# Optimization experiments

Measured on AMD Instinct MI355X. Metric: run time of the kernel, lower is better.

## Reference

```python
import jax, jax.numpy as jnp
import numpy as np

H = 256          # hidden_dim
E = 2 * H        # encoder output / attention embed dim = 512
MEL = 512        # mel_dim (must equal E for the original attention call to type-check)
NH = 8
HD = E // NH     # 64
B = 16
T = 128
V = 256          # vocab_size
NSPK = 100       # hardcoded speaker embedding rows
MAX_LEN = min(1000, T * 10)  # 1000 decode steps


def setup_inputs() -> dict:
    key = jax.random.key(0)
    ks = iter(jax.random.split(key, 40))

    def w(shape, s=0.05):
        return jax.random.normal(next(ks), shape, dtype=jnp.float32) * s

    return {
        'text_tokens': jax.random.randint(next(ks), (B, T), 0, V),
        'speaker_id': jax.random.randint(next(ks), (B,), 0, NSPK),
        'emb_text': w((V, H)),
        'emb_speaker': w((NSPK, H)),
        # bidirectional encoder LSTM (PyTorch gate order i,f,g,o)
        'enc_f_Wih': w((4 * H, H)), 'enc_f_Whh': w((4 * H, H)),
        'enc_f_bih': w((4 * H,)), 'enc_f_bhh': w((4 * H,)),
        'enc_b_Wih': w((4 * H, H)), 'enc_b_Whh': w((4 * H, H)),
        'enc_b_bih': w((4 * H,)), 'enc_b_bhh': w((4 * H,)),
        # multihead attention in/out projections
        'Wq': w((E, E)), 'bq': w((E,)),
        'Wk': w((E, E)), 'bk': w((E,)),
        'Wv': w((E, E)), 'bv': w((E,)),
        'Wo': w((E, E)), 'bo': w((E,)),
        # decoder LSTM (input dim = E + MEL); hidden state is re-zeroed every
        # step in the original (output state discarded), so Whh never acts.
        'dec_Wih': w((4 * H, E + MEL)), 'dec_Whh': w((4 * H, H)),
        'dec_bih': w((4 * H,)), 'dec_bhh': w((4 * H,)),
        'Wmel': w((MEL, H)), 'bmel': w((MEL,)),
        'Wstop': w((1, H)), 'bstop': w((1,)),
    }


def _lstm(x, Wih, Whh, bih, bhh, reverse=False):
    # x: [B, T, D] -> hidden sequence [B, T, H]
    Bx = x.shape[0]
    Hh = Whh.shape[1]
    h0 = jnp.zeros((Bx, Hh), x.dtype)

    def step(carry, xt):
        h, c = carry
        gates = xt @ Wih.T + bih + h @ Whh.T + bhh
        i, f, g, o = jnp.split(gates, 4, axis=-1)
        c = jax.nn.sigmoid(f) * c + jax.nn.sigmoid(i) * jnp.tanh(g)
        h = jax.nn.sigmoid(o) * jnp.tanh(c)
        return (h, c), h

    _, hs = jax.lax.scan(step, (h0, h0), jnp.swapaxes(x, 0, 1), reverse=reverse)
    return jnp.swapaxes(hs, 0, 1)


def reference(text_tokens, speaker_id, emb_text, emb_speaker,
              enc_f_Wih, enc_f_Whh, enc_f_bih, enc_f_bhh,
              enc_b_Wih, enc_b_Whh, enc_b_bih, enc_b_bhh,
              Wq, bq, Wk, bk, Wv, bv, Wo, bo,
              dec_Wih, dec_Whh, dec_bih, dec_bhh,
              Wmel, bmel, Wstop, bstop):
    # text + speaker embedding
    x = emb_text[text_tokens] + emb_speaker[speaker_id][:, None, :]   # [B,T,H]
    # bidirectional LSTM encoder
    enc_f = _lstm(x, enc_f_Wih, enc_f_Whh, enc_f_bih, enc_f_bhh)
    enc_b = _lstm(x, enc_b_Wih, enc_b_Whh, enc_b_bih, enc_b_bhh, reverse=True)
    enc = jnp.concatenate([enc_f, enc_b], axis=-1)                    # [B,T,E]

    # K/V projections are constant across decode steps -> hoist out of the loop
    K = (enc @ Wk.T + bk).reshape(B, T, NH, HD).transpose(0, 2, 1, 3)   # [B,NH,T,HD]
    Vv = (enc @ Wv.T + bv).reshape(B, T, NH, HD).transpose(0, 2, 1, 3)  # [B,NH,T,HD]
    scale = 1.0 / np.sqrt(HD).astype(np.float32)

    def step(mel_in, _):
        # single-query multihead attention (query = previous mel frame)
        q = (mel_in @ Wq.T + bq).reshape(B, NH, HD)                     # [B,NH,HD]
        w = jax.nn.softmax(jnp.einsum('bhd,bhtd->bht', q, K) * scale, axis=-1)
        ctx = jnp.einsum('bht,bhtd->bhd', w, Vv).reshape(B, E)
        attended = ctx @ Wo.T + bo                                      # [B,E]
        xin = jnp.concatenate([attended, mel_in], axis=-1)              # [B,E+MEL]
        # decoder LSTM single step from ZERO state each step (state discarded
        # in the original), so Whh term vanishes
        gates = xin @ dec_Wih.T + dec_bih + dec_bhh
        i, f, g, o = jnp.split(gates, 4, axis=-1)
        c = jax.nn.sigmoid(i) * jnp.tanh(g)
        h = jax.nn.sigmoid(o) * jnp.tanh(c)                             # [B,H]
        mel = h @ Wmel.T + bmel                                         # [B,MEL]
        stop = h @ Wstop.T + bstop                                      # [B,1]
        return mel, (mel, stop, w.mean(axis=1))

    mel0 = jnp.zeros((B, MEL), jnp.float32)
    _, (mels, stops, attns) = jax.lax.scan(step, mel0, None, length=MAX_LEN)

    mel_output = jnp.swapaxes(mels, 0, 1)    # [B,MAX_LEN,MEL]
    stop_output = jnp.swapaxes(stops, 0, 1)  # [B,MAX_LEN,1]
    attn_last = attns[-1][:, None, :]        # [B,1,T] (head-averaged, last step)
    return mel_output, stop_output, attn_last
```

## Files before the change

### kernel.cpp

```cpp
#include <hip/hip_runtime.h>
#include <hip/hip_bf16.h>


typedef unsigned short u16;
typedef unsigned int   u32;
#define DI __device__ __forceinline__

static constexpr size_t WS_BAR   = 0;
static constexpr size_t WS_GBUF  = 64*1024;
static constexpr size_t WS_HBUF  = 192*1024;
static constexpr size_t WS_PROBS = 208*1024;
static constexpr size_t WS_BIAS  = 272*1024;
static constexpr size_t WS_W2M   = 320*1024;
static constexpr size_t WS_WQH   = 832*1024;
static constexpr size_t WS_WCG   = 1344*1024;

static constexpr size_t OF_ENC_A = 262144;
static constexpr size_t OF_ENC_B = 1286144;
static constexpr size_t OF_XWF   = 4015744;
static constexpr size_t OF_XWB   = 6112896;

DI float bf2f(u16 u){ union{u32 i; float f;} v; v.i = ((u32)u)<<16; return v.f; }
DI u16 f2bf(float f){ union{float f; u32 i;} v; v.f = f;
  u32 r = v.i + 0x7fffu + ((v.i>>16)&1u); return (u16)(r>>16); }
DI float2 bf2x(u32 u){ union{u32 i; float f;} a,b; a.i = u<<16; b.i = u & 0xffff0000u;
  float2 r; r.x = a.f; r.y = b.f; return r; }
DI float dot8(uint4 wv, float4 a, float4 b){
  float2 w0 = bf2x(wv.x), w1 = bf2x(wv.y), w2 = bf2x(wv.z), w3 = bf2x(wv.w);
  return w0.x*a.x + w0.y*a.y + w1.x*a.z + w1.y*a.w
       + w2.x*b.x + w2.y*b.y + w3.x*b.z + w3.y*b.w;
}
DI float dot8f(float4 wa, float4 wb, float4 a, float4 b){
  return wa.x*a.x + wa.y*a.y + wa.z*a.z + wa.w*a.w
       + wb.x*b.x + wb.y*b.y + wb.z*b.z + wb.w*b.w;
}
DI float sigm(float x){ return 1.f/(1.f + __expf(-x)); }

DI float afload(const float* p){
  return __hip_atomic_load(p, __ATOMIC_RELAXED, __HIP_MEMORY_SCOPE_AGENT);
}
DI void afstore(float* p, float v){
  __hip_atomic_store(p, v, __ATOMIC_RELAXED, __HIP_MEMORY_SCOPE_AGENT);
}
DI void aadd(float* p, float v){
  __hip_atomic_fetch_add(p, v, __ATOMIC_RELAXED, __HIP_MEMORY_SCOPE_AGENT);
}

DI void bar_arrive(int* flags, int myidx, int t){
  __syncthreads();
  if (threadIdx.x == 0){
    __builtin_amdgcn_s_waitcnt(0);
    __hip_atomic_store(flags + myidx*32, t, __ATOMIC_RELAXED, __HIP_MEMORY_SCOPE_AGENT);
  }
}
DI void bar_wait(int* flags, int n, int t){
  if (threadIdx.x < 64){
    const int idx = threadIdx.x & (n-1);
    int v = __hip_atomic_load(flags + idx*32, __ATOMIC_RELAXED, __HIP_MEMORY_SCOPE_AGENT);
    while (__any(v < t)){
      __builtin_amdgcn_s_sleep(1);
      if (v < t)
        v = __hip_atomic_load(flags + idx*32, __ATOMIC_RELAXED, __HIP_MEMORY_SCOPE_AGENT);
    }
  }
  __asm__ __volatile__("" ::: "memory");
  __syncthreads();
}

__global__ __launch_bounds__(256) void k_init(int* bars, float* hbuf){
  const int i = blockIdx.x*256 + threadIdx.x;
  for (int k = i; k < 49152; k += 32*256) bars[k] = 0;
  if (i < 4096) hbuf[i] = 0.f;
}

__global__ __launch_bounds__(256) void k_xw(
    const int* __restrict__ tok, const int* __restrict__ spk,
    const float* __restrict__ et, const float* __restrict__ es,
    const float* __restrict__ WihF, const float* __restrict__ bihF, const float* __restrict__ bhhF,
    const float* __restrict__ WihB, const float* __restrict__ bihB, const float* __restrict__ bhhB,
    float* __restrict__ xwf, float* __restrict__ xwb){
  const int tid = threadIdx.x, bi = blockIdx.x;
  const int dir = bi & 1, jc = (bi >> 1) & 3, btg = bi >> 3;
  const int j = jc*256 + tid;
  const float* W = (dir ? WihB : WihF) + j*256;
  const float bias = (dir ? bihB : bihF)[j] + (dir ? bhhB : bhhF)[j];
  float* xw = dir ? xwb : xwf;

  __shared__ __align__(16) float lx[8][256];
  #pragma unroll
  for (int r = 0; r < 8; ++r){
    const int bt = btg*8 + r;
    lx[r][tid] = et[tok[bt]*256 + tid] + es[spk[bt>>7]*256 + tid];
  }
  __syncthreads();

  float acc[8];
  #pragma unroll
  for (int k2 = 0; k2 < 8; ++k2) acc[k2] = bias;
  for (int h = 0; h < 256; h += 8){
    float4 w0 = *(const float4*)(W + h);
    float4 w1 = *(const float4*)(W + h + 4);
    #pragma unroll
    for (int k2 = 0; k2 < 8; ++k2)
      acc[k2] += dot8f(w0, w1, *(const float4*)(&lx[k2][h]), *(const float4*)(&lx[k2][h+4]));
  }
  #pragma unroll
  for (int k2 = 0; k2 < 8; ++k2) xw[(btg*8 + k2)*1024 + j] = acc[k2];
}

__global__ __launch_bounds__(256) void k_fuse(
    const float* __restrict__ decW, const float* __restrict__ Wo,
    const float* __restrict__ Wmel, const float* __restrict__ Wq,
    u16* __restrict__ Wcg, u16* __restrict__ W2m, float* __restrict__ Wqh){
  const int tid = threadIdx.x, blk = blockIdx.x;
  float acc[4] = {0.f,0.f,0.f,0.f};
  if (blk < 512){
    const int g0 = (blk >> 1)*4, e = (blk & 1)*256 + tid;
    for (int jj = 0; jj < 512; ++jj){
      float wo = Wo[jj*512 + e];
      #pragma unroll
      for (int i2 = 0; i2 < 4; ++i2) acc[i2] += decW[(g0+i2)*1024 + jj] * wo;
    }
    #pragma unroll
    for (int i2 = 0; i2 < 4; ++i2) Wcg[(g0+i2)*512 + e] = f2bf(acc[i2]);
  } else if (blk < 768){
    const int g0 = (blk - 512)*4, h = tid;
    for (int m = 0; m < 512; ++m){
      float wm = Wmel[m*256 + h];
      #pragma unroll
      for (int i2 = 0; i2 < 4; ++i2) acc[i2] += decW[(g0+i2)*1024 + 512 + m] * wm;
    }
    #pragma unroll
    for (int i2 = 0; i2 < 4; ++i2) W2m[(g0+i2)*256 + h] = f2bf(acc[i2]);
  } else {
    const int j0 = (blk - 768)*4, h = tid;
    for (int e = 0; e < 512; ++e){
      float wm = Wmel[e*256 + h];
      #pragma unroll
      for (int i2 = 0; i2 < 4; ++i2) acc[i2] += Wq[(j0+i2)*512 + e] * wm;
    }
    #pragma unroll
    for (int i2 = 0; i2 < 4; ++i2) Wqh[(j0+i2)*256 + h] = acc[i2];
  }
}

__global__ __launch_bounds__(256) void k_bias(
    const float* __restrict__ Wq, const float* __restrict__ bq, const float* __restrict__ bmel,
    const float* __restrict__ decW, const float* __restrict__ bo,
    const float* __restrict__ bih, const float* __restrict__ bhh, float* __restrict__ biasws){
  const int o = blockIdx.x*256 + threadIdx.x;
  if (o < 512){
    float s = bq[o];
    for (int e = 0; e < 512; ++e) s += Wq[o*512 + e] * bmel[e];
    biasws[o] = s;
  } else {
    const int gr = o - 512;
    float s1 = bih[gr] + bhh[gr];
    for (int jj = 0; jj < 512; ++jj) s1 += decW[gr*1024 + jj] * bo[jj];
    biasws[512 + gr] = s1;
    float s2 = s1;
    for (int m = 0; m < 512; ++m) s2 += decW[gr*1024 + 512 + m] * bmel[m];
    biasws[1536 + gr] = s2;
  }
}

__global__ __launch_bounds__(128) void k_enc(
    const float* __restrict__ xwf, const float* __restrict__ xwb,
    const float* __restrict__ WhhF, const float* __restrict__ WhhB,
    float* encA, float* encB, int* bars){
  const int tid = threadIdx.x;
  const int xcd = blockIdx.x & 7, sl = blockIdx.x >> 3;
  const int grp = xcd*4 + (sl >> 3);
  const int w = sl & 7;
  const int dir = grp & 1, b = grp >> 1;
  int* bar = bars + (16 + grp)*1024;
  const float* Whh = dir ? WhhB : WhhF;
  const float* xw = dir ? xwb : xwf;
  float* encb = (b < 8 ? encA : encB) + (size_t)(b & 7)*65536;
  const int q = tid >> 5, ii = tid & 31;
  const int j = q*256 + w*32 + ii;
  const float* wr = Whh + j*256;

  __shared__ __align__(16) float l_h[256];
  __shared__ float l_g[4][32];
  __shared__ float l_c[32];
  if (tid < 32) l_c[tid] = 0.f;
  __syncthreads();

  for (int it = 0; it < 128; ++it){
    const int ts = dir ? (127 - it) : it;
    float acc = xw[(b*128 + ts)*1024 + j];
    if (it > 0){
      const int tp = dir ? (ts + 1) : (ts - 1);
      const float* hp = encb + tp*512 + dir*256;
      for (int i = tid; i < 256; i += 128) l_h[i] = afload(hp + i);
      __syncthreads();
      #pragma unroll 4
      for (int k = 0; k < 256; k += 8)
        acc += dot8f(*(const float4*)(wr + k), *(const float4*)(wr + k + 4),
                     *(const float4*)(&l_h[k]), *(const float4*)(&l_h[k + 4]));
    }
    l_g[q][ii] = acc;
    __syncthreads();
    if (tid < 32){
      float ig = l_g[0][tid], fg = l_g[1][tid], gg = l_g[2][tid], og = l_g[3][tid];
      float c = sigm(fg)*l_c[tid] + sigm(ig)*tanhf(gg);
      l_c[tid] = c;
      afstore(encb + ts*512 + dir*256 + w*32 + tid, sigm(og)*tanhf(c));
    }
    bar_arrive(bar, w, it+1);
    bar_wait(bar, 8, it+1);
  }
}

__global__ __launch_bounds__(256) void k_proj(
    const float* __restrict__ encA, const float* __restrict__ encB,
    const float* __restrict__ Wk, const float* __restrict__ bk,
    const float* __restrict__ Wv, const float* __restrict__ bv,
    float* outf){
  const int tid = threadIdx.x, x = blockIdx.x;
  const int role = x & 1, dc = (x >> 1) & 1, btg = x >> 2;
  const int row = dc*256 + tid;
  const float* W = (role ? Wv : Wk) + row*512;
  const float bias = (role ? bv : bk)[row];
  const int b = (btg*8) >> 7;
  const float* eb = (b < 8 ? encA : encB) + (size_t)(b & 7)*65536;
  float acc[8];
  #pragma unroll
  for (int k2 = 0; k2 < 8; ++k2) acc[k2] = bias;
  for (int e = 0; e < 512; e += 8){
    float4 wa = *(const float4*)(W + e);
    float4 wb = *(const float4*)(W + e + 4);
    #pragma unroll
    for (int k2 = 0; k2 < 8; ++k2){
      const float* ep = eb + ((btg*8 + k2) & 127)*512 + e;
      acc[k2] += dot8f(wa, wb, *(const float4*)(ep), *(const float4*)(ep + 4));
    }
  }
  const int head = row >> 6, dd = row & 63;
  float* kv = outf + (size_t)(b >> 1)*1024000 + (size_t)(b & 1)*131072;
  #pragma unroll
  for (int k2 = 0; k2 < 8; ++k2){
    const int ts = (btg*8 + k2) & 127;
    if (role == 0) kv[head*8192 + ts*64 + dd] = acc[k2];
    else           kv[65536 + head*8192 + dd*128 + ts] = acc[k2];
  }
}

__global__ __launch_bounds__(512) void k_decode(
    const float* __restrict__ Wqh,
    const u16*   __restrict__ Wcg,
    const u16*   __restrict__ W2m,
    const float* __restrict__ Wmel,
    const float* __restrict__ bmel,
    const float* __restrict__ Wstop, const float* __restrict__ bstop,
    const float* __restrict__ bq,
    const float* __restrict__ biasws,
    float* Gbuf,
    float* probs, int* bars,
    float* out){
  const int tid = threadIdx.x;
  const int b = blockIdx.x & 15, sidx = blockIdx.x >> 4;
  const int h = sidx >> 1, half = sidx & 1;
  const int d = tid & 63, ko = tid >> 6;
  int* bflag = bars + b*512;
  float* out_mel  = out;
  float* out_stop = out + 8192000;
  float* out_attn = out + 8208000;

  __shared__ __align__(16) float lK[128*68];
  __shared__ __align__(16) u16  lWV[384*136];
  __shared__ __align__(16) float l_h[256];
  __shared__ __align__(16) float l_hw[8*36];
  __shared__ __align__(16) float l_q[64];
  __shared__ __align__(16) float l_p[128];
  __shared__ __align__(16) float l_qt[8][64];
  __shared__ float l_r[4];

  const float* kv = out + (size_t)(b >> 1)*1024000 + (size_t)(b & 1)*131072;
  const int rg = tid >> 2, c4 = tid & 3;
  const int rw = tid >> 3, c8 = tid & 7;
  const int r2 = half*384 + h*48 + rw;

  {
    const float* gV = kv + 65536 + h*8192;
    for (int i = tid; i < 8192; i += 512){
      const int dd = i >> 7, t = i & 127;
      lK[t*68 + dd] = gV[i];
    }
  }
  __syncthreads();
  {
    #pragma unroll
    for (int s = 0; s < 3; ++s){
      const int rloc = rg*3 + s;
      const int rpk  = half*384 + rloc;
      const int orig = rpk + (rpk >= 256 ? 256 : 0);
      const u16* wp = Wcg + orig*512 + h*64;
      uint4 w0 = *(const uint4*)(wp),      w1 = *(const uint4*)(wp + 8);
      uint4 w2_ = *(const uint4*)(wp + 16), w3 = *(const uint4*)(wp + 24);
      uint4 w4 = *(const uint4*)(wp + 32), w5 = *(const uint4*)(wp + 40);
      uint4 w6 = *(const uint4*)(wp + 48), w7 = *(const uint4*)(wp + 56);
      for (int jj = 0; jj < 32; ++jj){
        const int t = c4*32 + ((jj + 2*c4) & 31);
        const float4* vv = (const float4*)(lK + t*68);
        float acc = dot8(w0, vv[0], vv[1])  + dot8(w1, vv[2], vv[3])
                  + dot8(w2_, vv[4], vv[5]) + dot8(w3, vv[6], vv[7])
                  + dot8(w4, vv[8], vv[9])  + dot8(w5, vv[10], vv[11])
                  + dot8(w6, vv[12], vv[13])+ dot8(w7, vv[14], vv[15]);
        lWV[rloc*136 + t] = f2bf(acc);
      }
    }
  }
  __syncthreads();
  {
    const float* gK = kv + h*8192;
    for (int i = tid; i < 2048; i += 512){
      const int r = i >> 4, c = i & 15;
      *(float4*)(lK + r*68 + c*4) = *(const float4*)(gK + r*64 + c*4);
    }
  }

  float4 wq[8];
  {
    const float* p = Wqh + (h*64 + d)*256 + ko*32;
    #pragma unroll
    for (int j = 0; j < 8; ++j) wq[j] = *(const float4*)(p + 4*j);
  }
  uint4 w2[4];
  {
    const int orig2 = r2 + (r2 >= 256 ? 256 : 0);
    const u16* p = W2m + (tid < 384 ? orig2*256 + c8*32 : 0);
    #pragma unroll
    for (int j = 0; j < 4; ++j) w2[j] = *(const uint4*)(p + 8*j);
  }
  const float bq0 = bq[h*64 + d];
  const float bq1 = biasws[h*64 + d];
  const float bmd = bmel[h*64 + (tid >> 6)*8 + ((tid & 63) >> 3)];
  float bgi0=0, bgg0=0, bgo0=0, bgi1=0, bgg1=0, bgo1=0;
  if (tid < 256){
    bgi0 = biasws[ 512 + tid]; bgg0 = biasws[1024 + tid]; bgo0 = biasws[1280 + tid];
    bgi1 = biasws[1536 + tid]; bgg1 = biasws[2048 + tid]; bgo1 = biasws[2304 + tid];
  }
  float4 wst4 = {0.f,0.f,0.f,0.f};
  if (h == 0 && half == 0 && tid < 64) wst4 = *(const float4*)(Wstop + tid*4);
  const float bst = bstop[0];

  if (tid < 256) l_h[tid] = 0.f;
  if (tid < 288) l_hw[tid] = 0.f;
  float hreg = 0.f;
  __syncthreads();

  int rot = 0;
  for (int t = 0; t < 1000; ++t){
    float* buf = Gbuf + (rot*16 + b)*768;
    {
      const float4* hh = (const float4*)(l_h + ko*32);
      l_qt[ko][d] = dot8f(wq[0], wq[1], hh[0], hh[1]) + dot8f(wq[2], wq[3], hh[2], hh[3])
                  + dot8f(wq[4], wq[5], hh[4], hh[5]) + dot8f(wq[6], wq[7], hh[6], hh[7]);
    }
    if (tid < 384){
      const float4* hh = (const float4*)(l_hw + c8*36);
      float w2p = dot8(w2[0], hh[0], hh[1]) + dot8(w2[1], hh[2], hh[3])
                + dot8(w2[2], hh[4], hh[5]) + dot8(w2[3], hh[6], hh[7]);
      w2p += __shfl_xor(w2p, 1);
      w2p += __shfl_xor(w2p, 2);
      w2p += __shfl_xor(w2p, 4);
      if (c8 == 0) aadd(buf + r2, w2p);
    }
    __syncthreads();
    if (tid < 64){
      float qq = (t == 0 ? bq0 : bq1);
      #pragma unroll
      for (int k = 0; k < 8; ++k) qq += l_qt[k][tid];
      l_q[tid] = qq;
      __asm__ __volatile__("s_waitcnt lgkmcnt(0)" ::: "memory");
      const float* kr0 = lK + tid*68;
      const float* kr1 = lK + (tid + 64)*68;
      float s0 = 0.f, s1 = 0.f;
      #pragma unroll
      for (int k = 0; k < 64; k += 8){
        float4 qa = *(const float4*)(l_q + k), qb = *(const float4*)(l_q + k + 4);
        s0 += dot8f(*(const float4*)(kr0 + k), *(const float4*)(kr0 + k + 4), qa, qb);
        s1 += dot8f(*(const float4*)(kr1 + k), *(const float4*)(kr1 + k + 4), qa, qb);
      }
      s0 *= 0.125f; s1 *= 0.125f;
      float m = fmaxf(s0, s1);
      #pragma unroll
      for (int off = 32; off; off >>= 1) m = fmaxf(m, __shfl_xor(m, off));
      float p0 = __expf(s0 - m), p1 = __expf(s1 - m);
      float ss = p0 + p1;
      #pragma unroll
      for (int off = 32; off; off >>= 1) ss += __shfl_xor(ss, off);
      l_p[tid] = p0; l_p[tid + 64] = p1;
      if (tid == 0){ l_r[0] = ss; l_r[1] = 1.f/ss; }
    }
    __syncthreads();
    if (tid < 384){
      const float invS = l_r[1];
      const u16* wr = lWV + tid*136;
      const float4* pp = (const float4*)l_p;
      float acc = 0.f;
      #pragma unroll 4
      for (int k = 0; k < 16; ++k)
        acc += dot8(*(const uint4*)(wr + 8*k), pp[2*k], pp[2*k+1]);
      aadd(buf + half*384 + tid, acc*invS);
    }
    if (t >= 2 && tid >= 464){
      int rr = rot + 1; if (rr == 3) rr = 0;
      afstore(Gbuf + (rr*16 + b)*768 + sidx*48 + (tid - 464), 0.f);
    }
    bar_arrive(bflag, sidx, t+1);
    if (t == 1) bar_wait(bars + (b ^ 1)*512, 16, 1);
    if (half == 0 && t > 0){
      const int ln = tid & 63;
      const int dd = (tid >> 6)*8 + (ln >> 3), cc = ln & 7;
      const float* pm = Wmel + (h*64 + dd)*256 + cc*32;
      const float4* hh = (const float4*)(l_hw + cc*36);
      float mp = dot8f(*(const float4*)(pm),      *(const float4*)(pm + 4),  hh[0], hh[1])
               + dot8f(*(const float4*)(pm + 8),  *(const float4*)(pm + 12), hh[2], hh[3])
               + dot8f(*(const float4*)(pm + 16), *(const float4*)(pm + 20), hh[4], hh[5])
               + dot8f(*(const float4*)(pm + 24), *(const float4*)(pm + 28), hh[6], hh[7]);
      mp += __shfl_xor(mp, 1); mp += __shfl_xor(mp, 2); mp += __shfl_xor(mp, 4);
      if (cc == 0) out_mel[((size_t)b*1000 + (t-1))*512 + h*64 + dd] = mp + bmd;
      if (h == 0 && tid < 64){
        const float4 h4v = *(const float4*)(l_h + tid*4);
        float sp = wst4.x*h4v.x + wst4.y*h4v.y + wst4.z*h4v.z + wst4.w*h4v.w;
        #pragma unroll
        for (int off = 32; off; off >>= 1) sp += __shfl_xor(sp, off);
        if (tid == 0) out_stop[b*1000 + (t-1)] = sp + bst;
      }
    }
    bar_wait(bflag, 16, t+1);
    if (tid < 256){
      float gi = (t == 0 ? bgi0 : bgi1) + afload(buf + tid);
      float gg = (t == 0 ? bgg0 : bgg1) + afload(buf + 256 + tid);
      float go = (t == 0 ? bgo0 : bgo1) + afload(buf + 512 + tid);
      float c = sigm(gi) * tanhf(gg);
      hreg = sigm(go) * tanhf(c);
      l_h[tid] = hreg;
      l_hw[(tid >> 5)*36 + (tid & 31)] = hreg;
    }
    __syncthreads();
    rot = (rot == 2) ? 0 : rot + 1;
  }

  if (half == 0){
    const int ln = tid & 63;
    const int dd = (tid >> 6)*8 + (ln >> 3), cc = ln & 7;
    const float* pm = Wmel + (h*64 + dd)*256 + cc*32;
    const float4* hh = (const float4*)(l_hw + cc*36);
    float mp = dot8f(*(const float4*)(pm),      *(const float4*)(pm + 4),  hh[0], hh[1])
             + dot8f(*(const float4*)(pm + 8),  *(const float4*)(pm + 12), hh[2], hh[3])
             + dot8f(*(const float4*)(pm + 16), *(const float4*)(pm + 20), hh[4], hh[5])
             + dot8f(*(const float4*)(pm + 24), *(const float4*)(pm + 28), hh[6], hh[7]);
    mp += __shfl_xor(mp, 1); mp += __shfl_xor(mp, 2); mp += __shfl_xor(mp, 4);
    if (cc == 0) out_mel[((size_t)b*1000 + 999)*512 + h*64 + dd] = mp + bmd;
    if (h == 0 && tid < 64){
      const float4 h4v = *(const float4*)(l_h + tid*4);
      float sp = wst4.x*h4v.x + wst4.y*h4v.y + wst4.z*h4v.z + wst4.w*h4v.w;
      #pragma unroll
      for (int off = 32; off; off >>= 1) sp += __shfl_xor(sp, off);
      if (tid == 0) out_stop[b*1000 + 999] = sp + bst;
    }
    if (tid < 128)
      afstore(probs + (b*8 + h)*128 + tid, l_p[tid] / l_r[0]);
  }
  bar_arrive(bflag, sidx, 1001);
  if (h == 0 && half == 0){
    bar_wait(bflag, 16, 1001);
    if (tid < 128){
      float ssum = 0.f;
      #pragma unroll
      for (int hh = 0; hh < 8; ++hh) ssum += afload(probs + (b*8 + hh)*128 + tid);
      out_attn[b*128 + tid] = ssum * 0.125f;
    }
  }
}

extern "C" void kernel_launch(void* const* d_in, const int* in_sizes, int n_in,
                              void* d_out, int out_size, void* d_ws, size_t ws_size,
                              hipStream_t stream){
  const int*   tok = (const int*)d_in[0];
  const int*   spk = (const int*)d_in[1];
  const float* emb_text = (const float*)d_in[2];
  const float* emb_spk  = (const float*)d_in[3];
  const float* WihF = (const float*)d_in[4];
  const float* WhhF = (const float*)d_in[5];
  const float* bihF = (const float*)d_in[6];
  const float* bhhF = (const float*)d_in[7];
  const float* WihB = (const float*)d_in[8];
  const float* WhhB = (const float*)d_in[9];
  const float* bihB = (const float*)d_in[10];
  const float* bhhB = (const float*)d_in[11];
  const float* Wq = (const float*)d_in[12];
  const float* bq = (const float*)d_in[13];
  const float* Wk = (const float*)d_in[14];
  const float* bk = (const float*)d_in[15];
  const float* Wv = (const float*)d_in[16];
  const float* bv = (const float*)d_in[17];
  const float* Wo = (const float*)d_in[18];
  const float* bo = (const float*)d_in[19];
  const float* decW = (const float*)d_in[20];
  const float* bih = (const float*)d_in[22];
  const float* bhh = (const float*)d_in[23];
  const float* Wmel = (const float*)d_in[24];
  const float* bmel = (const float*)d_in[25];
  const float* Wstop = (const float*)d_in[26];
  const float* bstop = (const float*)d_in[27];

  char* ws = (char*)d_ws;
  int*   bars   = (int*)(ws + WS_BAR);
  float* Gbuf   = (float*)(ws + WS_GBUF);
  float* hbuf   = (float*)(ws + WS_HBUF);
  float* probs  = (float*)(ws + WS_PROBS);
  float* biasws = (float*)(ws + WS_BIAS);
  u16*   W2m    = (u16*)(ws + WS_W2M);
  float* Wqh    = (float*)(ws + WS_WQH);
  u16*   Wcg    = (u16*)(ws + WS_WCG);

  float* outf = (float*)d_out;
  float* encA = outf + OF_ENC_A;
  float* encB = outf + OF_ENC_B;
  float* xwf  = outf + OF_XWF;
  float* xwb  = outf + OF_XWB;

  k_init <<<32,   256, 0, stream>>>(bars, hbuf);
  k_xw   <<<2048, 256, 0, stream>>>(tok, spk, emb_text, emb_spk,
                                    WihF, bihF, bhhF, WihB, bihB, bhhB, xwf, xwb);
  k_enc  <<<256,  128, 0, stream>>>(xwf, xwb, WhhF, WhhB, encA, encB, bars);
  k_fuse <<<896,  256, 0, stream>>>(decW, Wo, Wmel, Wq, Wcg, W2m, Wqh);
  k_bias <<<6,    256, 0, stream>>>(Wq, bq, bmel, decW, bo, bih, bhh, biasws);
  k_proj <<<1024, 256, 0, stream>>>(encA, encB, Wk, bk, Wv, bv, outf);
  k_decode<<<256, 512, 0, stream>>>(Wqh, Wcg, W2m, Wmel, bmel, Wstop, bstop,
                                    bq, biasws, Gbuf, probs, bars, outf);
}
```

Baseline: 6.947 ms.

## Compute per-head context first, then project through Wcg held in registers

Drops the prologue that precomputed a bf16 Wcg·V matrix (384x128) in shared memory. Each step now forms the 64-wide attention context from fp32 V held in LDS and multiplies it by Wcg slices kept in registers, which cuts per-step LDS traffic and the startup work. The mel projection is split across both half-blocks so each does 32 rows instead of one half doing all 64, and the Gbuf zeroing moves to otherwise idle threads. The cost is a serial 128-long context dot product per thread inside the softmax section and more register pressure.

```diff
diff --git a/kernel.cpp b/kernel.cpp
--- a/kernel.cpp
+++ b/kernel.cpp
@@ -269,56 +269,31 @@
   float* out_attn = out + 8208000;
 
   __shared__ __align__(16) float lK[128*68];
-  __shared__ __align__(16) u16  lWV[384*136];
+  __shared__ __align__(16) float lV[64*132];
   __shared__ __align__(16) float l_h[256];
   __shared__ __align__(16) float l_hw[8*36];
   __shared__ __align__(16) float l_q[64];
   __shared__ __align__(16) float l_p[128];
+  __shared__ __align__(16) float l_ct[64];
   __shared__ __align__(16) float l_qt[8][64];
-  __shared__ float l_r[4];
+  __shared__ float l_r[2];
 
   const float* kv = out + (size_t)(b >> 1)*1024000 + (size_t)(b & 1)*131072;
   const int rg = tid >> 2, c4 = tid & 3;
   const int rw = tid >> 3, c8 = tid & 7;
   const int r2 = half*384 + h*48 + rw;
 
-  {
-    const float* gV = kv + 65536 + h*8192;
-    for (int i = tid; i < 8192; i += 512){
-      const int dd = i >> 7, t = i & 127;
-      lK[t*68 + dd] = gV[i];
-    }
-  }
-  __syncthreads();
-  {
-    #pragma unroll
-    for (int s = 0; s < 3; ++s){
-      const int rloc = rg*3 + s;
-      const int rpk  = half*384 + rloc;
-      const int orig = rpk + (rpk >= 256 ? 256 : 0);
-      const u16* wp = Wcg + orig*512 + h*64;
-      uint4 w0 = *(const uint4*)(wp),      w1 = *(const uint4*)(wp + 8);
-      uint4 w2_ = *(const uint4*)(wp + 16), w3 = *(const uint4*)(wp + 24);
-      uint4 w4 = *(const uint4*)(wp + 32), w5 = *(const uint4*)(wp + 40);
-      uint4 w6 = *(const uint4*)(wp + 48), w7 = *(const uint4*)(wp + 56);
-      for (int jj = 0; jj < 32; ++jj){
-        const int t = c4*32 + ((jj + 2*c4) & 31);
-        const float4* vv = (const float4*)(lK + t*68);
-        float acc = dot8(w0, vv[0], vv[1])  + dot8(w1, vv[2], vv[3])
-                  + dot8(w2_, vv[4], vv[5]) + dot8(w3, vv[6], vv[7])
-                  + dot8(w4, vv[8], vv[9])  + dot8(w5, vv[10], vv[11])
-                  + dot8(w6, vv[12], vv[13])+ dot8(w7, vv[14], vv[15]);
-        lWV[rloc*136 + t] = f2bf(acc);
-      }
-    }
-  }
-  __syncthreads();
   {
     const float* gK = kv + h*8192;
     for (int i = tid; i < 2048; i += 512){
       const int r = i >> 4, c = i & 15;
       *(float4*)(lK + r*68 + c*4) = *(const float4*)(gK + r*64 + c*4);
     }
+    const float* gV = kv + 65536 + h*8192;
+    for (int i = tid; i < 2048; i += 512){
+      const int r = i >> 5, c = i & 31;
+      *(float4*)(lV + r*132 + c*4) = *(const float4*)(gV + r*128 + c*4);
+    }
   }
 
   float4 wq[8];
@@ -326,6 +301,15 @@
     const float* p = Wqh + (h*64 + d)*256 + ko*32;
     #pragma unroll
     for (int j = 0; j < 8; ++j) wq[j] = *(const float4*)(p + 4*j);
+  }
+  uint4 wcg[3][2];
+  #pragma unroll
+  for (int s = 0; s < 3; ++s){
+    const int r = half*384 + rg*3 + s;
+    const int orig = r + (r >= 256 ? 256 : 0);
+    const u16* p = Wcg + orig*512 + h*64 + c4*16;
+    wcg[s][0] = *(const uint4*)(p);
+    wcg[s][1] = *(const uint4*)(p + 8);
   }
   uint4 w2[4];
   {
@@ -336,14 +320,14 @@
   }
   const float bq0 = bq[h*64 + d];
   const float bq1 = biasws[h*64 + d];
-  const float bmd = bmel[h*64 + (tid >> 6)*8 + ((tid & 63) >> 3)];
+  const float bmd = bmel[h*64 + half*32 + ((tid & 255) >> 3)];
   float bgi0=0, bgg0=0, bgo0=0, bgi1=0, bgg1=0, bgo1=0;
   if (tid < 256){
     bgi0 = biasws[ 512 + tid]; bgg0 = biasws[1024 + tid]; bgo0 = biasws[1280 + tid];
     bgi1 = biasws[1536 + tid]; bgg1 = biasws[2048 + tid]; bgo1 = biasws[2304 + tid];
   }
   float4 wst4 = {0.f,0.f,0.f,0.f};
-  if (h == 0 && half == 0 && tid < 64) wst4 = *(const float4*)(Wstop + tid*4);
+  if (h == 0 && half == 1 && tid < 64) wst4 = *(const float4*)(Wstop + tid*4);
   const float bst = bstop[0];
 
   if (tid < 256) l_h[tid] = 0.f;
@@ -367,6 +351,9 @@
       w2p += __shfl_xor(w2p, 2);
       w2p += __shfl_xor(w2p, 4);
       if (c8 == 0) aadd(buf + r2, w2p);
+    } else if (t >= 2 && tid >= 432 && tid < 480){
+      int rr = rot + 1; if (rr == 3) rr = 0;
+      afstore(Gbuf + (rr*16 + b)*768 + sidx*48 + (tid - 432), 0.f);
     }
     __syncthreads();
     if (tid < 64){
@@ -393,37 +380,48 @@
       #pragma unroll
       for (int off = 32; off; off >>= 1) ss += __shfl_xor(ss, off);
       l_p[tid] = p0; l_p[tid + 64] = p1;
-      if (tid == 0){ l_r[0] = ss; l_r[1] = 1.f/ss; }
+      __asm__ __volatile__("s_waitcnt lgkmcnt(0)" ::: "memory");
+      const float* vr = lV + tid*132;
+      float cs = 0.f;
+      #pragma unroll
+      for (int k = 0; k < 128; k += 8)
+        cs += dot8f(*(const float4*)(vr + k), *(const float4*)(vr + k + 4),
+                    *(const float4*)(l_p + k), *(const float4*)(l_p + k + 4));
+      l_ct[tid] = cs / ss;
+      if (tid == 0) l_r[0] = ss;
     }
     __syncthreads();
-    if (tid < 384){
-      const float invS = l_r[1];
-      const u16* wr = lWV + tid*136;
-      const float4* pp = (const float4*)l_p;
-      float acc = 0.f;
-      #pragma unroll 4
-      for (int k = 0; k < 16; ++k)
-        acc += dot8(*(const uint4*)(wr + 8*k), pp[2*k], pp[2*k+1]);
-      aadd(buf + half*384 + tid, acc*invS);
-    }
-    if (t >= 2 && tid >= 464){
-      int rr = rot + 1; if (rr == 3) rr = 0;
-      afstore(Gbuf + (rr*16 + b)*768 + sidx*48 + (tid - 464), 0.f);
+    {
+      const float4* ct = (const float4*)(l_ct + c4*16);
+      float4 c0 = ct[0], c1 = ct[1], c2 = ct[2], c3 = ct[3];
+      float pr0 = dot8(wcg[0][0], c0, c1) + dot8(wcg[0][1], c2, c3);
+      float pr1 = dot8(wcg[1][0], c0, c1) + dot8(wcg[1][1], c2, c3);
+      float pr2 = dot8(wcg[2][0], c0, c1) + dot8(wcg[2][1], c2, c3);
+      pr0 += __shfl_xor(pr0, 1); pr0 += __shfl_xor(pr0, 2);
+      pr1 += __shfl_xor(pr1, 1); pr1 += __shfl_xor(pr1, 2);
+      pr2 += __shfl_xor(pr2, 1); pr2 += __shfl_xor(pr2, 2);
+      if (c4 == 0){
+        const int rb = half*384 + rg*3;
+        aadd(buf + rb,     pr0);
+        aadd(buf + rb + 1, pr1);
+        aadd(buf + rb + 2, pr2);
+      }
     }
     bar_arrive(bflag, sidx, t+1);
     if (t == 1) bar_wait(bars + (b ^ 1)*512, 16, 1);
-    if (half == 0 && t > 0){
-      const int ln = tid & 63;
-      const int dd = (tid >> 6)*8 + (ln >> 3), cc = ln & 7;
-      const float* pm = Wmel + (h*64 + dd)*256 + cc*32;
-      const float4* hh = (const float4*)(l_hw + cc*36);
-      float mp = dot8f(*(const float4*)(pm),      *(const float4*)(pm + 4),  hh[0], hh[1])
-               + dot8f(*(const float4*)(pm + 8),  *(const float4*)(pm + 12), hh[2], hh[3])
-               + dot8f(*(const float4*)(pm + 16), *(const float4*)(pm + 20), hh[4], hh[5])
-               + dot8f(*(const float4*)(pm + 24), *(const float4*)(pm + 28), hh[6], hh[7]);
-      mp += __shfl_xor(mp, 1); mp += __shfl_xor(mp, 2); mp += __shfl_xor(mp, 4);
-      if (cc == 0) out_mel[((size_t)b*1000 + (t-1))*512 + h*64 + dd] = mp + bmd;
-      if (h == 0 && tid < 64){
+    if (t > 0){
+      if (tid < 256){
+        const int dd = half*32 + (tid >> 3), cc = tid & 7;
+        const float* pm = Wmel + (h*64 + dd)*256 + cc*32;
+        const float4* hh = (const float4*)(l_hw + cc*36);
+        float mp = dot8f(*(const float4*)(pm),      *(const float4*)(pm + 4),  hh[0], hh[1])
+                 + dot8f(*(const float4*)(pm + 8),  *(const float4*)(pm + 12), hh[2], hh[3])
+                 + dot8f(*(const float4*)(pm + 16), *(const float4*)(pm + 20), hh[4], hh[5])
+                 + dot8f(*(const float4*)(pm + 24), *(const float4*)(pm + 28), hh[6], hh[7]);
+        mp += __shfl_xor(mp, 1); mp += __shfl_xor(mp, 2); mp += __shfl_xor(mp, 4);
+        if (cc == 0) out_mel[((size_t)b*1000 + (t-1))*512 + h*64 + dd] = mp + bmd;
+      }
+      if (h == 0 && half == 1 && tid < 64){
         const float4 h4v = *(const float4*)(l_h + tid*4);
         float sp = wst4.x*h4v.x + wst4.y*h4v.y + wst4.z*h4v.z + wst4.w*h4v.w;
         #pragma unroll
@@ -445,9 +443,8 @@
     rot = (rot == 2) ? 0 : rot + 1;
   }
 
-  if (half == 0){
-    const int ln = tid & 63;
-    const int dd = (tid >> 6)*8 + (ln >> 3), cc = ln & 7;
+  if (tid < 256){
+    const int dd = half*32 + (tid >> 3), cc = tid & 7;
     const float* pm = Wmel + (h*64 + dd)*256 + cc*32;
     const float4* hh = (const float4*)(l_hw + cc*36);
     float mp = dot8f(*(const float4*)(pm),      *(const float4*)(pm + 4),  hh[0], hh[1])
@@ -456,16 +453,16 @@
              + dot8f(*(const float4*)(pm + 24), *(const float4*)(pm + 28), hh[6], hh[7]);
     mp += __shfl_xor(mp, 1); mp += __shfl_xor(mp, 2); mp += __shfl_xor(mp, 4);
     if (cc == 0) out_mel[((size_t)b*1000 + 999)*512 + h*64 + dd] = mp + bmd;
-    if (h == 0 && tid < 64){
-      const float4 h4v = *(const float4*)(l_h + tid*4);
-      float sp = wst4.x*h4v.x + wst4.y*h4v.y + wst4.z*h4v.z + wst4.w*h4v.w;
-      #pragma unroll
-      for (int off = 32; off; off >>= 1) sp += __shfl_xor(sp, off);
-      if (tid == 0) out_stop[b*1000 + 999] = sp + bst;
-    }
-    if (tid < 128)
-      afstore(probs + (b*8 + h)*128 + tid, l_p[tid] / l_r[0]);
-  }
+  }
+  if (h == 0 && half == 1 && tid < 64){
+    const float4 h4v = *(const float4*)(l_h + tid*4);
+    float sp = wst4.x*h4v.x + wst4.y*h4v.y + wst4.z*h4v.z + wst4.w*h4v.w;
+    #pragma unroll
+    for (int off = 32; off; off >>= 1) sp += __shfl_xor(sp, off);
+    if (tid == 0) out_stop[b*1000 + 999] = sp + bst;
+  }
+  if (half == 0 && tid < 128)
+    afstore(probs + (b*8 + h)*128 + tid, l_p[tid] / l_r[0]);
   bar_arrive(bflag, sidx, 1001);
   if (h == 0 && half == 0){
     bar_wait(bflag, 16, 1001);
```

Result: faster. 6.617 ms (median of 2 runs) (-4.8%).
